# Performance work log

Measured on AMD Instinct MI355X. Metric: run time of the kernel, lower is better.

The kernel has to match this reference:

```python
import jax, jax.numpy as jnp
import numpy as np

N = 50000; E = 800000; G = 64
HID = 128; HEADS = 4; HC = HID // HEADS
L = 3; RESID_FREQ = 2
EPS = 1e-5; SLOPE = 0.2


def setup_inputs() -> dict:
    key = jax.random.key(0)
    ks = jax.random.split(key, 16)
    s = 1.0 / np.sqrt(HID)
    f = jnp.float32
    return {
        "x": jax.random.normal(ks[0], (N, HID), f),
        "edge_index": jax.random.randint(ks[1], (2, E), 0, N, dtype=jnp.int32),
        "batch": jnp.sort(jax.random.randint(ks[2], (N,), 0, G, dtype=jnp.int32)),
        "w_in1": jax.random.normal(ks[3], (HID, HID), f) * s,
        "b_in1": jnp.zeros((HID,), f),
        "w_in2": jax.random.normal(ks[4], (HID, HID), f) * s,
        "b_in2": jnp.zeros((HID,), f),
        "gat_w": jax.random.normal(ks[5], (L, HID, HID), f) * s,
        "gat_att_src": jax.random.normal(ks[6], (L, HEADS, HC), f) * s,
        "gat_att_dst": jax.random.normal(ks[7], (L, HEADS, HC), f) * s,
        "gat_b": jnp.zeros((L, HID), f),
        "gcn_w": jax.random.normal(ks[8], (L, HID, HID), f) * s,
        "gcn_b": jnp.zeros((L, HID), f),
        "norm_w": jnp.ones((L, HID), f),
        "norm_b": jnp.zeros((L, HID), f),
        "norm_ms": jnp.ones((L, HID), f),
        "skip_w": jax.random.normal(ks[9], (L, HID, HID), f) * s,
        "skip_b": jnp.zeros((L, HID), f),
        "w_h1": jax.random.normal(ks[10], (HID, HID), f) * s,
        "b_h1": jnp.zeros((HID,), f),
        "w_h2": jax.random.normal(ks[11], (HID, HID // 2), f) * s,
        "b_h2": jnp.zeros((HID // 2,), f),
        "w_h3": jax.random.normal(ks[12], (HID // 2, 1), f) * s,
        "b_h3": jnp.zeros((1,), f),
        "edge_w_param": jnp.ones((1,), f),
    }


def _gat(x, src, dst, w, a_src, a_dst, b):
    # PyG GATConv (eval): lin -> per-edge additive attention -> edge softmax over dst -> scatter-sum
    h = (x @ w).reshape(N, HEADS, HC)
    sc_src = jnp.sum(h * a_src, axis=-1)  # [N, H]
    sc_dst = jnp.sum(h * a_dst, axis=-1)
    alpha = jax.nn.leaky_relu(sc_src[src] + sc_dst[dst], SLOPE)  # [Ef, H]
    amax = jax.ops.segment_max(alpha, dst, num_segments=N)  # every node has a self-loop
    ex = jnp.exp(alpha - amax[dst])
    denom = jax.ops.segment_sum(ex, dst, num_segments=N)
    coef = ex / (denom[dst] + 1e-16)
    out = jax.ops.segment_sum(h[src] * coef[:, :, None], dst, num_segments=N)
    return out.reshape(N, HID) + b


def _gcn(x, src, dst, ew, w, b):
    # PyG GCNConv with improved=True (self-loop weight 2.0 already in ew): sym-normalized SpMM
    deg = jax.ops.segment_sum(ew, dst, num_segments=N)
    dinv = jnp.where(deg > 0, jax.lax.rsqrt(deg), 0.0)
    norm = dinv[src] * ew * dinv[dst]
    h = x @ w
    return jax.ops.segment_sum(h[src] * norm[:, None], dst, num_segments=N) + b


def _graph_norm(x, batch, w, b, ms):
    cnt = jax.ops.segment_sum(jnp.ones((N, 1), x.dtype), batch, num_segments=G)
    cnt = jnp.maximum(cnt, 1.0)
    mean = jax.ops.segment_sum(x, batch, num_segments=G) / cnt
    out = x - mean[batch] * ms
    var = jax.ops.segment_sum(out * out, batch, num_segments=G) / cnt
    return out / jnp.sqrt(var[batch] + EPS) * w + b


def reference(x, edge_index, batch, w_in1, b_in1, w_in2, b_in2, gat_w, gat_att_src,
              gat_att_dst, gat_b, gcn_w, gcn_b, norm_w, norm_b, norm_ms, skip_w,
              skip_b, w_h1, b_h1, w_h2, b_h2, w_h3, b_h3, edge_w_param):
    # undirected: concat reversed edges; then self-loops (added by both GAT and GCN convs)
    loop = jnp.arange(N, dtype=edge_index.dtype)
    src = jnp.concatenate([edge_index[0], edge_index[1], loop])
    dst = jnp.concatenate([edge_index[1], edge_index[0], loop])
    ew = jnp.concatenate([
        edge_w_param[0] * jnp.ones((2 * E,), x.dtype),
        2.0 * jnp.ones((N,), x.dtype),  # improved=True self-loop fill value
    ])
    h = jax.nn.relu(x @ w_in1 + b_in1) @ w_in2 + b_in2
    for i in range(L):
        prev = h
        g1 = _gat(h, src, dst, gat_w[i], gat_att_src[i], gat_att_dst[i], gat_b[i])
        g2 = _gcn(h, src, dst, ew, gcn_w[i], gcn_b[i])
        h = jax.nn.elu(_graph_norm(g1 + g2, batch, norm_w[i], norm_b[i], norm_ms[i]))
        if i % RESID_FREQ == 0:
            h = h + prev @ skip_w[i] + skip_b[i]
    p = jax.nn.relu(h @ w_h1 + b_h1)
    p = jax.nn.relu(p @ w_h2 + b_h2)
    return jax.nn.sigmoid(p @ w_h3 + b_h3).reshape(-1)
```

## Files before the change

### kernel.cpp

```cpp
#include <hip/hip_runtime.h>
#include <hip/hip_fp16.h>

typedef unsigned int uint;
typedef unsigned short ushort;
typedef __attribute__((ext_vector_type(8))) short short8;
typedef __attribute__((ext_vector_type(4))) float f32x4;

#define N_NODES 50000
#define N_EDGES 800000
#define ETOT    (2 * N_EDGES + N_NODES)
#define NG      64
#define NBKT    256
#define MAXB    10240
#define EPB     8192
#define NBK1    ((ETOT + EPB - 1) / EPB)
#define GSTR    320

__device__ __forceinline__ short f2bf(float f) {
  uint u = __float_as_uint(f);
  u += 0x7fffu + ((u >> 16) & 1u);
  return (short)(u >> 16);
}
__device__ __forceinline__ float bf2f(short s) {
  return __uint_as_float(((uint)(ushort)s) << 16);
}
__device__ __forceinline__ uint packbf(float a, float b) {
  return (uint)(ushort)f2bf(a) | ((uint)(ushort)f2bf(b) << 16);
}
__device__ __forceinline__ uint pkh2(float a, float b) {
  __half2 h = __floats2half2_rn(a, b);
  return *(uint*)&h;
}
__device__ __forceinline__ float2 uph2(uint u) {
  __half2 h = *(__half2*)&u;
  return __half22float2(h);
}

__global__ __launch_bounds__(256) void bucket_k(const int* __restrict__ ei,
                                                int* __restrict__ gfill,
                                                uint* __restrict__ est) {
  __shared__ int hist[NBKT];
  __shared__ int cursor[NBKT];
  const int tid = threadIdx.x;
  hist[tid] = 0;
  __syncthreads();
  const int e0 = blockIdx.x * EPB;
#pragma unroll 4
  for (int i = 0; i < EPB / 256; ++i) {
    int e = e0 + i * 256 + tid;
    if (e < ETOT) {
      int d;
      if (e < N_EDGES)          d = ei[N_EDGES + e];
      else if (e < 2 * N_EDGES) d = ei[e - N_EDGES];
      else                      d = e - 2 * N_EDGES;
      atomicAdd(&hist[d >> 8], 1);
    }
  }
  __syncthreads();
  cursor[tid] = atomicAdd(&gfill[tid], hist[tid]);
  __syncthreads();
#pragma unroll 4
  for (int i = 0; i < EPB / 256; ++i) {
    int e = e0 + i * 256 + tid;
    if (e < ETOT) {
      int s, d, fl = 0;
      if (e < N_EDGES)          { s = ei[e];           d = ei[N_EDGES + e]; }
      else if (e < 2 * N_EDGES) { s = ei[e];           d = ei[e - N_EDGES]; }
      else                      { s = e - 2 * N_EDGES; d = s; fl = 1; }
      int b = d >> 8;
      int slot = atomicAdd(&cursor[b], 1);
      est[(size_t)b * MAXB + slot] = (uint)s | ((uint)(d & 255) << 16) | ((uint)fl << 24);
    }
  }
}

__global__ __launch_bounds__(256) void bktscan_k(const int* __restrict__ gfill,
                                                 int* __restrict__ bktbase) {
  __shared__ int wsum[4];
  int tid = threadIdx.x, lane = tid & 63, wid = tid >> 6;
  int v = gfill[tid];
  int x = v;
#pragma unroll
  for (int d = 1; d < 64; d <<= 1) {
    int t = __shfl_up(x, d, 64);
    if (lane >= d) x += t;
  }
  if (lane == 63) wsum[wid] = x;
  __syncthreads();
  int woff = 0;
#pragma unroll
  for (int j = 0; j < 4; ++j) if (j < wid) woff += wsum[j];
  bktbase[tid] = woff + x - v;
}

__global__ __launch_bounds__(256) void group_k(const int* __restrict__ gfill,
                                               const int* __restrict__ bktbase,
                                               const uint* __restrict__ est,
                                               const float* __restrict__ ewp,
                                               int* __restrict__ csrc,
                                               int* __restrict__ rbeg,
                                               int* __restrict__ rend,
                                               float* __restrict__ dinv) {
  __shared__ int hist[NBKT];
  __shared__ int cursor[NBKT];
  __shared__ int wsum[4];
  const int b = blockIdx.x;
  const int tid = threadIdx.x;
  const int cnt = gfill[b];
  const int gb = bktbase[b];
  hist[tid] = 0;
  __syncthreads();
  const uint* basep = est + (size_t)b * MAXB;
  for (int i = tid; i < cnt; i += 256)
    atomicAdd(&hist[(basep[i] >> 16) & 255], 1);
  __syncthreads();
  int v = hist[tid];
  int lane = tid & 63, wid = tid >> 6;
  int x = v;
#pragma unroll
  for (int d = 1; d < 64; d <<= 1) {
    int t = __shfl_up(x, d, 64);
    if (lane >= d) x += t;
  }
  if (lane == 63) wsum[wid] = x;
  __syncthreads();
  int woff = 0;
#pragma unroll
  for (int j = 0; j < 4; ++j) if (j < wid) woff += wsum[j];
  int excl = woff + x - v;
  cursor[tid] = excl;
  int node = b * 256 + tid;
  if (node < N_NODES) {
    rbeg[node] = gb + excl;
    rend[node] = gb + excl + v;
    float deg = ewp[0] * (float)(v - 1) + 2.0f;
    dinv[node] = (deg > 0.f) ? rsqrtf(deg) : 0.f;
  }
  __syncthreads();
  for (int i = tid; i < cnt; i += 256) {
    uint en = basep[i];
    int dlow = (en >> 16) & 255;
    int slot = atomicAdd(&cursor[dlow], 1);
    csrc[gb + slot] = (int)(en & 0xffffu) | (int)((en >> 24) << 31);
  }
}

__global__ __launch_bounds__(128) void gcnt_k(const int* __restrict__ batch,
                                              int* __restrict__ gcnt) {
  __shared__ int lb[NG + 1];
  int g = threadIdx.x;
  if (g <= NG) {
    int lo = 0, hi = N_NODES;
    while (lo < hi) {
      int mid = (lo + hi) >> 1;
      if (batch[mid] < g) lo = mid + 1; else hi = mid;
    }
    lb[g] = lo;
  }
  __syncthreads();
  if (g < NG) gcnt[g] = lb[g + 1] - lb[g];
}

__global__ __launch_bounds__(256) void convx_k(const float* __restrict__ x,
                                               short* __restrict__ xb) {
  int i = (blockIdx.x * 256 + threadIdx.x) * 4;
  float4 v = *(const float4*)(x + i);
  *(uint2*)(xb + i) = make_uint2(packbf(v.x, v.y), packbf(v.z, v.w));
}

__global__ __launch_bounds__(256) void prep_k(const float* __restrict__ w_in1,
                                              const float* __restrict__ w_in2,
                                              const float* __restrict__ gat_w,
                                              const float* __restrict__ gcn_w,
                                              const float* __restrict__ skip_w,
                                              const float* __restrict__ w_h1,
                                              const float* __restrict__ w_h2,
                                              short* __restrict__ WT0,
                                              short* __restrict__ WT1,
                                              short* __restrict__ WTL2,
                                              short* __restrict__ WTS,
                                              short* __restrict__ WTH1,
                                              short* __restrict__ WTH2) {
  int mat = blockIdx.x >> 2, qr = blockIdx.x & 3;
  const float* src; short* dst; int ncol = 128, dstride = 128, doff = 0;
  switch (mat) {
    case 0:  src = w_in1; dst = WT0; break;
    case 1:  src = w_in2; dst = WT1; break;
    case 2: case 3: case 4:
      src = gat_w + (size_t)(mat - 2) * 16384; dst = WTL2 + (size_t)(mat - 2) * 32768;
      dstride = 256; break;
    case 5: case 6: case 7:
      src = gcn_w + (size_t)(mat - 5) * 16384; dst = WTL2 + (size_t)(mat - 5) * 32768;
      dstride = 256; doff = 128; break;
    case 8:  src = skip_w;             dst = WTS;         break;
    case 9:  src = skip_w + 2 * 16384; dst = WTS + 16384; break;
    case 10: src = w_h1; dst = WTH1; break;
    default: src = w_h2; dst = WTH2; ncol = 64; break;
  }
  int total = 128 * ncol, chunk = total / 4;
  for (int d = qr * chunk + threadIdx.x; d < (qr + 1) * chunk; d += 256) {
    int col = d >> 7, k = d & 127;
    dst[col * dstride + doff + k] = f2bf(src[k * ncol + col]);
  }
}

__global__ __launch_bounds__(256) void attprep_k(const float* __restrict__ gat_w,
                                                 const float* __restrict__ asrc,
                                                 const float* __restrict__ adst,
                                                 const float* __restrict__ gat_b,
                                                 const float* __restrict__ gcn_b,
                                                 short* __restrict__ ATTW,
                                                 float* __restrict__ BSUM) {
  const int tid = threadIdx.x;
  for (int t = tid; t < 3072; t += 256) {
    int l = t >> 10, rem = t & 1023;
    int r = rem >> 7, k = rem & 127;
    int hd = r & 3;
    const float* av = (r < 4) ? (asrc + l * 128 + hd * 32) : (adst + l * 128 + hd * 32);
    const float* wrow = gat_w + (size_t)l * 16384 + k * 128 + hd * 32;
    float s = 0.f;
#pragma unroll
    for (int c = 0; c < 32; ++c) s = fmaf(wrow[c], av[c], s);
    ATTW[(size_t)l * 2048 + r * 128 + k] = f2bf(s);
  }
  for (int t = tid; t < 3072; t += 256)
    ATTW[(size_t)(t >> 10) * 2048 + 1024 + (t & 1023)] = 0;
  for (int t = tid; t < 384; t += 256) {
    int l = t >> 7, c = t & 127;
    BSUM[t] = gat_b[l * 128 + c] + gcn_b[l * 128 + c];
  }
}

template <int NCOL, int RELU, int ADD, int F32OUT>
__global__ __launch_bounds__(256) void bgemm_k(const short* __restrict__ A,
                                               const short* __restrict__ WT,
                                               const float* __restrict__ bias,
                                               const float* __restrict__ addsrc,
                                               short* __restrict__ outb,
                                               float* __restrict__ outf,
                                               int astr, int M) {
  constexpr int NT = NCOL / 16;
  const int lane = threadIdx.x & 63;
  const int wid = threadIdx.x >> 6;
  const int mbase = blockIdx.x * 64 + wid * 16;
  const int l15 = lane & 15, q = lane >> 4;
  int arow = mbase + l15; if (arow > M - 1) arow = M - 1;
  const short* ap = A + (size_t)arow * 128 + q * 8;
  const short* bp = WT + (size_t)l15 * 128 + q * 8;
  f32x4 acc[NT];
#pragma unroll
  for (int t = 0; t < NT; ++t) acc[t] = (f32x4)0.f;
#pragma unroll
  for (int c = 0; c < 4; ++c) {
    short8 av = *(const short8*)(ap + c * 32);
#pragma unroll
    for (int t = 0; t < NT; ++t) {
      short8 bv = *(const short8*)(bp + (size_t)t * 16 * 128 + c * 32);
      acc[t] = __builtin_amdgcn_mfma_f32_16x16x32_bf16(av, bv, acc[t], 0, 0, 0);
    }
  }
#pragma unroll
  for (int t = 0; t < NT; ++t) {
    int col = t * 16 + l15;
    float bb = bias ? bias[col] : 0.f;
#pragma unroll
    for (int r = 0; r < 4; ++r) {
      int row = mbase + q * 4 + r;
      if (row < M) {
        float v = acc[t][r] + bb;
        if (ADD) v += addsrc[(size_t)row * astr + col];
        if (RELU) v = v > 0.f ? v : 0.f;
        if (F32OUT) outf[(size_t)row * NCOL + col] = v;
        else        outb[(size_t)row * NCOL + col] = f2bf(v);
      }
    }
  }
}

__global__ __launch_bounds__(256) void coef_k(const float* __restrict__ sc,
                                              const int* __restrict__ rbeg,
                                              const int* __restrict__ rend,
                                              const int* __restrict__ cs,
                                              const float* __restrict__ dinv,
                                              const float* __restrict__ ewp,
                                              uint* __restrict__ COEF) {
  const int n = blockIdx.x * 4 + (threadIdx.x >> 6);
  const int l = threadIdx.x & 63;
  const float ew0 = ewp[0];
  const float dn = dinv[n];
  const f32x4 sdv = *(const f32x4*)(sc + n * 16 + 4);
  const int beg = rbeg[n], end = rend[n];
  float den0 = 0.f, den1 = 0.f, den2 = 0.f, den3 = 0.f;
  for (int e = beg + l; e < end; e += 64) {
    int raw = cs[e];
    int s = raw & 0x7fffffff;
    float w = (raw < 0) ? 2.0f : ew0;
    f32x4 ssv = *(const f32x4*)(sc + (size_t)s * 16);
    float a0 = ssv[0] + sdv[0]; a0 = fmaxf(a0, 0.2f * a0);
    float a1 = ssv[1] + sdv[1]; a1 = fmaxf(a1, 0.2f * a1);
    float a2 = ssv[2] + sdv[2]; a2 = fmaxf(a2, 0.2f * a2);
    float a3 = ssv[3] + sdv[3]; a3 = fmaxf(a3, 0.2f * a3);
    float e0 = __expf(a0), e1 = __expf(a1), e2 = __expf(a2), e3 = __expf(a3);
    den0 += e0; den1 += e1; den2 += e2; den3 += e3;
    float c2 = dinv[s] * w * dn;
    uint* cp = COEF + (size_t)e * 3;
    cp[0] = pkh2(e0, e1);
    cp[1] = pkh2(e2, e3);
    __half hc = __float2half(c2);
    cp[2] = (uint)(*(ushort*)&hc) | ((uint)s << 16);
  }
#pragma unroll
  for (int off = 32; off; off >>= 1) {
    den0 += __shfl_xor(den0, off, 64);
    den1 += __shfl_xor(den1, off, 64);
    den2 += __shfl_xor(den2, off, 64);
    den3 += __shfl_xor(den3, off, 64);
  }
  float i0 = 1.0f / (den0 + 1e-16f), i1 = 1.0f / (den1 + 1e-16f);
  float i2 = 1.0f / (den2 + 1e-16f), i3 = 1.0f / (den3 + 1e-16f);
  for (int e = beg + l; e < end; e += 64) {
    uint* cp = COEF + (size_t)e * 3;
    float2 p01 = uph2(cp[0]);
    float2 p23 = uph2(cp[1]);
    cp[0] = pkh2(p01.x * i0, p01.y * i1);
    cp[1] = pkh2(p23.x * i2, p23.y * i3);
  }
}

__global__ __launch_bounds__(256) void agg_k(const short* __restrict__ h,
                                             const uint* __restrict__ COEF,
                                             const int* __restrict__ rbeg,
                                             const int* __restrict__ rend,
                                             short* __restrict__ A) {
  const int n = blockIdx.x * 4 + (threadIdx.x >> 6);
  const int l = threadIdx.x & 63;
  const int sub = l >> 5;
  const int f4 = l & 31;
  const int beg = rbeg[n], end = rend[n];
  float ag[4][4], ac[4];
#pragma unroll
  for (int hd = 0; hd < 4; ++hd)
#pragma unroll
    for (int i = 0; i < 4; ++i) ag[hd][i] = 0.f;
#pragma unroll
  for (int i = 0; i < 4; ++i) ac[i] = 0.f;
  for (int e0 = beg; e0 < end; e0 += 2) {
    int e = e0 + sub;
    int ec = (e < end) ? e : ETOT;
    const uint* cp = COEF + (size_t)ec * 3;
    uint c0 = cp[0], c1 = cp[1], c2w = cp[2];
    int s = (int)(c2w >> 16);
    float2 p01 = uph2(c0);
    float2 p23 = uph2(c1);
    ushort hc = (ushort)(c2w & 0xffffu);
    float c2 = __half2float(*(__half*)&hc);
    uint2 u = *(const uint2*)(h + (size_t)s * 128 + f4 * 4);
    float v0 = __uint_as_float(u.x << 16);
    float v1 = __uint_as_float(u.x & 0xffff0000u);
    float v2 = __uint_as_float(u.y << 16);
    float v3 = __uint_as_float(u.y & 0xffff0000u);
    ag[0][0] = fmaf(p01.x, v0, ag[0][0]); ag[0][1] = fmaf(p01.x, v1, ag[0][1]);
    ag[0][2] = fmaf(p01.x, v2, ag[0][2]); ag[0][3] = fmaf(p01.x, v3, ag[0][3]);
    ag[1][0] = fmaf(p01.y, v0, ag[1][0]); ag[1][1] = fmaf(p01.y, v1, ag[1][1]);
    ag[1][2] = fmaf(p01.y, v2, ag[1][2]); ag[1][3] = fmaf(p01.y, v3, ag[1][3]);
    ag[2][0] = fmaf(p23.x, v0, ag[2][0]); ag[2][1] = fmaf(p23.x, v1, ag[2][1]);
    ag[2][2] = fmaf(p23.x, v2, ag[2][2]); ag[2][3] = fmaf(p23.x, v3, ag[2][3]);
    ag[3][0] = fmaf(p23.y, v0, ag[3][0]); ag[3][1] = fmaf(p23.y, v1, ag[3][1]);
    ag[3][2] = fmaf(p23.y, v2, ag[3][2]); ag[3][3] = fmaf(p23.y, v3, ag[3][3]);
    ac[0] = fmaf(c2, v0, ac[0]); ac[1] = fmaf(c2, v1, ac[1]);
    ac[2] = fmaf(c2, v2, ac[2]); ac[3] = fmaf(c2, v3, ac[3]);
  }
#pragma unroll
  for (int hd = 0; hd < 4; ++hd)
#pragma unroll
    for (int i = 0; i < 4; ++i) ag[hd][i] += __shfl_xor(ag[hd][i], 32);
#pragma unroll
  for (int i = 0; i < 4; ++i) ac[i] += __shfl_xor(ac[i], 32);
  short* base = A + (size_t)n * 640;
  if (sub == 0) {
#pragma unroll
    for (int hd = 0; hd < 2; ++hd) {
      *(uint2*)(base + hd * 128 + f4 * 4) =
          make_uint2(packbf(ag[hd][0], ag[hd][1]), packbf(ag[hd][2], ag[hd][3]));
    }
    *(uint2*)(base + 512 + f4 * 4) =
        make_uint2(packbf(ac[0], ac[1]), packbf(ac[2], ac[3]));
  } else {
#pragma unroll
    for (int hd = 2; hd < 4; ++hd) {
      *(uint2*)(base + hd * 128 + f4 * 4) =
          make_uint2(packbf(ag[hd][0], ag[hd][1]), packbf(ag[hd][2], ag[hd][3]));
    }
  }
}

__global__ __launch_bounds__(256) void aggproj_k(const short* A,
                                                 const short* __restrict__ WT,
                                                 const float* __restrict__ bsum,
                                                 float* G, int M) {
  const int lane = threadIdx.x & 63;
  const int wid = threadIdx.x >> 6;
  const int mbase = blockIdx.x * 64 + wid * 16;
  const int l15 = lane & 15, q = lane >> 4;
  int arow = mbase + l15; if (arow > M - 1) arow = M - 1;
  const short* ap = A + (size_t)arow * 640 + q * 8;
  const short* bp = WT + (size_t)l15 * 256 + q * 8;
  f32x4 acc[8];
#pragma unroll
  for (int t = 0; t < 8; ++t) acc[t] = (f32x4)0.f;
  short8 avg[4];
#pragma unroll
  for (int c = 0; c < 4; ++c) avg[c] = *(const short8*)(ap + 512 + c * 32);
#pragma unroll
  for (int hd = 0; hd < 4; ++hd) {
    short8 avh[4];
#pragma unroll
    for (int c = 0; c < 4; ++c) avh[c] = *(const short8*)(ap + hd * 128 + c * 32);
#pragma unroll
    for (int tt = 0; tt < 2; ++tt) {
      int t = hd * 2 + tt;
      const short* bpt = bp + (size_t)t * 16 * 256;
#pragma unroll
      for (int c = 0; c < 4; ++c) {
        short8 bv = *(const short8*)(bpt + c * 32);
        acc[t] = __builtin_amdgcn_mfma_f32_16x16x32_bf16(avh[c], bv, acc[t], 0, 0, 0);
      }
#pragma unroll
      for (int c = 0; c < 4; ++c) {
        short8 bv = *(const short8*)(bpt + 128 + c * 32);
        acc[t] = __builtin_amdgcn_mfma_f32_16x16x32_bf16(avg[c], bv, acc[t], 0, 0, 0);
      }
    }
  }
#pragma unroll
  for (int t = 0; t < 8; ++t) {
    int col = t * 16 + l15;
    float bb = bsum[col];
#pragma unroll
    for (int r = 0; r < 4; ++r) {
      int row = mbase + q * 4 + r;
      if (row < M) G[(size_t)row * GSTR + col] = acc[t][r] + bb;
    }
  }
}

__global__ __launch_bounds__(256) void stats_k(const float* __restrict__ g,
                                               const int* __restrict__ batch,
                                               float* __restrict__ gsum) {
  int c = threadIdx.x & 127;
  int half = threadIdx.x >> 7;
  int nb = blockIdx.x * 16;
  float s = 0.f, q = 0.f;
  int curb = -1;
  for (int i = half; i < 16; i += 2) {
    int n = nb + i;
    int b = batch[n];
    if (b != curb) {
      if (curb >= 0) {
        atomicAdd(&gsum[curb * 256 + c], s);
        atomicAdd(&gsum[curb * 256 + 128 + c], q);
      }
      curb = b; s = 0.f; q = 0.f;
    }
    float v = g[(size_t)n * GSTR + c];
    s += v;
    q = fmaf(v, v, q);
  }
  if (curb >= 0) {
    atomicAdd(&gsum[curb * 256 + c], s);
    atomicAdd(&gsum[curb * 256 + 128 + c], q);
  }
}

template <int OUTBF16>
__global__ __launch_bounds__(256) void normelu_k(float* __restrict__ g,
                                                 const int* __restrict__ batch,
                                                 const float* __restrict__ gsum,
                                                 const int* __restrict__ gcnt,
                                                 const float* __restrict__ nw,
                                                 const float* __restrict__ nb_,
                                                 const float* __restrict__ nms,
                                                 short* __restrict__ outb) {
  int n = blockIdx.x * 2 + (threadIdx.x >> 7);
  int c = threadIdx.x & 127;
  int b = batch[n];
  float cntf = fmaxf((float)gcnt[b], 1.0f);
  float inv = 1.0f / cntf;
  float mean = gsum[b * 256 + c] * inv;
  float msq  = gsum[b * 256 + 128 + c] * inv;
  float ms = nms[c];
  float var = fmaxf(msq - (2.0f * ms - ms * ms) * mean * mean, 0.f);
  float v = g[(size_t)n * GSTR + c];
  float o = (v - mean * ms) * rsqrtf(var + 1e-5f) * nw[c] + nb_[c];
  o = (o > 0.f) ? o : (__expf(o) - 1.0f);
  if (OUTBF16) outb[(size_t)n * 128 + c] = f2bf(o);
  else         g[(size_t)n * GSTR + c] = o;
}

__global__ __launch_bounds__(256) void head3_k(const short* __restrict__ p2,
                                               const float* __restrict__ w3,
                                               const float* __restrict__ b3,
                                               float* __restrict__ out) {
  int n = blockIdx.x * 4 + (threadIdx.x >> 6);
  int k = threadIdx.x & 63;
  float v = bf2f(p2[(size_t)n * 64 + k]) * w3[k];
#pragma unroll
  for (int off = 32; off; off >>= 1) v += __shfl_down(v, off, 64);
  if (k == 0) out[n] = 1.0f / (1.0f + __expf(-(v + b3[0])));
}

extern "C" void kernel_launch(void* const* d_in, const int* in_sizes, int n_in,
                              void* d_out, int out_size, void* d_ws, size_t ws_size,
                              hipStream_t stream) {
  const float* x      = (const float*)d_in[0];
  const int*   ei     = (const int*)d_in[1];
  const int*   batch  = (const int*)d_in[2];
  const float* w_in1  = (const float*)d_in[3];
  const float* b_in1  = (const float*)d_in[4];
  const float* w_in2  = (const float*)d_in[5];
  const float* b_in2  = (const float*)d_in[6];
  const float* gat_w  = (const float*)d_in[7];
  const float* gat_as = (const float*)d_in[8];
  const float* gat_ad = (const float*)d_in[9];
  const float* gat_b  = (const float*)d_in[10];
  const float* gcn_w  = (const float*)d_in[11];
  const float* gcn_b  = (const float*)d_in[12];
  const float* norm_w = (const float*)d_in[13];
  const float* norm_b = (const float*)d_in[14];
  const float* norm_ms= (const float*)d_in[15];
  const float* skip_w = (const float*)d_in[16];
  const float* skip_b = (const float*)d_in[17];
  const float* w_h1   = (const float*)d_in[18];
  const float* b_h1   = (const float*)d_in[19];
  const float* w_h2   = (const float*)d_in[20];
  const float* b_h2   = (const float*)d_in[21];
  const float* w_h3   = (const float*)d_in[22];
  const float* b_h3   = (const float*)d_in[23];
  const float* ewp    = (const float*)d_in[24];
  float* out = (float*)d_out;

  char* p = (char*)d_ws;
  const size_t NBH = (size_t)N_NODES * 128 * sizeof(short);
  short* B0   = (short*)p; p += NBH;
  short* B1   = (short*)p; p += NBH;
  short* MEGA = (short*)p; p += (size_t)N_NODES * 640 * sizeof(short);
  float* G    = (float*)MEGA;
  uint*  EST  = (uint*)MEGA;
  float* SC   = (float*)p; p += (size_t)N_NODES * 16 * sizeof(float);
  int*   CSRC = (int*)p;   p += (size_t)ETOT * sizeof(int);
  uint*  COEF = (uint*)p;  p += (size_t)(ETOT + 1) * 3 * sizeof(uint);
  int*   RBEG = (int*)p;   p += (size_t)N_NODES * sizeof(int);
  int*   REND = (int*)p;   p += (size_t)N_NODES * sizeof(int);
  char*  zbase = p;
  int*   GFILL= (int*)p;   p += (size_t)NBKT * sizeof(int);
  float* GSUM = (float*)p; p += (size_t)3 * NG * 256 * sizeof(float);
  size_t znb  = (size_t)((char*)p - zbase);
  int*   BKTB = (int*)p;   p += (size_t)NBKT * sizeof(int);
  int*   GCNT = (int*)p;   p += (size_t)NG * sizeof(int);
  float* DINV = (float*)p; p += (size_t)N_NODES * sizeof(float);
  short* WT0  = (short*)p; p += 16384 * sizeof(short);
  short* WT1  = (short*)p; p += 16384 * sizeof(short);
  short* WTL2 = (short*)p; p += 3 * 32768 * sizeof(short);
  short* WTS  = (short*)p; p += 2 * 16384 * sizeof(short);
  short* WTH1 = (short*)p; p += 16384 * sizeof(short);
  short* WTH2 = (short*)p; p += 8192 * sizeof(short);
  short* ATTW = (short*)p; p += 3 * 2048 * sizeof(short);
  float* BSUM = (float*)p; p += 3 * 128 * sizeof(float);

  const int GB = (N_NODES + 63) / 64;

  hipMemsetAsync(zbase, 0, znb, stream);
  hipMemsetAsync(COEF + (size_t)ETOT * 3, 0, 12, stream);
  bucket_k<<<NBK1, 256, 0, stream>>>(ei, GFILL, EST);
  bktscan_k<<<1, 256, 0, stream>>>(GFILL, BKTB);
  group_k<<<196, 256, 0, stream>>>(GFILL, BKTB, EST, ewp, CSRC, RBEG, REND, DINV);
  gcnt_k<<<1, 128, 0, stream>>>(batch, GCNT);
  convx_k<<<(N_NODES * 128) / 1024, 256, 0, stream>>>(x, B0);
  prep_k<<<48, 256, 0, stream>>>(w_in1, w_in2, gat_w, gcn_w, skip_w, w_h1, w_h2,
                                 WT0, WT1, WTL2, WTS, WTH1, WTH2);
  attprep_k<<<1, 256, 0, stream>>>(gat_w, gat_as, gat_ad, gat_b, gcn_b, ATTW, BSUM);

  bgemm_k<128, 1, 0, 0><<<GB, 256, 0, stream>>>(B0, WT0, b_in1, nullptr, B1, nullptr, 0, N_NODES);
  bgemm_k<128, 0, 0, 0><<<GB, 256, 0, stream>>>(B1, WT1, b_in2, nullptr, B0, nullptr, 0, N_NODES);

  short* h = B0;
  for (int i = 0; i < 3; ++i) {
    short* hn = (h == B0) ? B1 : B0;
    float* gsum_i = GSUM + (size_t)i * NG * 256;
    bgemm_k<16, 0, 0, 1><<<GB, 256, 0, stream>>>(h, ATTW + (size_t)i * 2048,
                                                 nullptr, nullptr, nullptr, SC, 0, N_NODES);
    coef_k<<<N_NODES / 4, 256, 0, stream>>>(SC, RBEG, REND, CSRC, DINV, ewp, COEF);
    agg_k<<<N_NODES / 4, 256, 0, stream>>>(h, COEF, RBEG, REND, MEGA);
    aggproj_k<<<GB, 256, 0, stream>>>(MEGA, WTL2 + (size_t)i * 32768,
                                      BSUM + i * 128, G, N_NODES);
    stats_k<<<N_NODES / 16, 256, 0, stream>>>(G, batch, gsum_i);
    if (i == 1) {
      normelu_k<1><<<N_NODES / 2, 256, 0, stream>>>(G, batch, gsum_i, GCNT,
          norm_w + (size_t)i * 128, norm_b + (size_t)i * 128, norm_ms + (size_t)i * 128,
          hn);
    } else {
      normelu_k<0><<<N_NODES / 2, 256, 0, stream>>>(G, batch, gsum_i, GCNT,
          norm_w + (size_t)i * 128, norm_b + (size_t)i * 128, norm_ms + (size_t)i * 128,
          nullptr);
      const short* wts = WTS + (size_t)(i == 0 ? 0 : 1) * 16384;
      bgemm_k<128, 0, 1, 0><<<GB, 256, 0, stream>>>(h, wts, skip_b + (size_t)i * 128,
                                                    G, hn, nullptr, GSTR, N_NODES);
    }
    h = hn;
  }

  bgemm_k<128, 1, 0, 0><<<GB, 256, 0, stream>>>(h, WTH1, b_h1, nullptr, B0, nullptr, 0, N_NODES);
  bgemm_k<64, 1, 0, 0><<<GB, 256, 0, stream>>>(B0, WTH2, b_h2, nullptr, MEGA, nullptr, 0, N_NODES);
  head3_k<<<N_NODES / 4, 256, 0, stream>>>(MEGA, w_h3, b_h3, out);
}
```

Measured before the change: 984.4 us.

## Fuse edge-coefficient computation into aggregation and store graph-norm intermediates in bf16

Merges the separate coef_k pass into agg_k: each wave computes unnormalized attention exponents and GCN weights for 64 edges at a time into shared memory, aggregates them, and applies the softmax denominator at the end. This removes the COEF global buffer and its write/read/rewrite traffic plus one launch per layer. The projected pre-norm output G also switches from fp32 to bf16, the normalized result goes to a separate bf16 buffer, and stats/normelu are widened to two channels per thread. The cost is some precision loss in the norm inputs and softmax exponents that are no longer max-subtracted, though the code before also skipped that subtraction.

Result: faster. 878.1 us (-10.8%).

```diff
diff --git a/kernel.cpp b/kernel.cpp
--- a/kernel.cpp
+++ b/kernel.cpp
@@ -14,7 +14,7 @@
 #define MAXB    10240
 #define EPB     8192
 #define NBK1    ((ETOT + EPB - 1) / EPB)
-#define GSTR    320
+#define AROW    640
 
 __device__ __forceinline__ short f2bf(float f) {
   uint u = __float_as_uint(f);
@@ -235,10 +235,9 @@
 __global__ __launch_bounds__(256) void bgemm_k(const short* __restrict__ A,
                                                const short* __restrict__ WT,
                                                const float* __restrict__ bias,
-                                               const float* __restrict__ addsrc,
+                                               const short* __restrict__ addsrc,
                                                short* __restrict__ outb,
-                                               float* __restrict__ outf,
-                                               int astr, int M) {
+                                               float* __restrict__ outf, int M) {
   constexpr int NT = NCOL / 16;
   const int lane = threadIdx.x & 63;
   const int wid = threadIdx.x >> 6;
@@ -268,7 +267,7 @@
       int row = mbase + q * 4 + r;
       if (row < M) {
         float v = acc[t][r] + bb;
-        if (ADD) v += addsrc[(size_t)row * astr + col];
+        if (ADD) v += bf2f(addsrc[(size_t)row * 128 + col]);
         if (RELU) v = v > 0.f ? v : 0.f;
         if (F32OUT) outf[(size_t)row * NCOL + col] = v;
         else        outb[(size_t)row * NCOL + col] = f2bf(v);
@@ -277,66 +276,25 @@
   }
 }
 
-__global__ __launch_bounds__(256) void coef_k(const float* __restrict__ sc,
-                                              const int* __restrict__ rbeg,
-                                              const int* __restrict__ rend,
-                                              const int* __restrict__ cs,
-                                              const float* __restrict__ dinv,
-                                              const float* __restrict__ ewp,
-                                              uint* __restrict__ COEF) {
+__global__ __launch_bounds__(256) void agg_k(const short* __restrict__ h,
+                                             const float* __restrict__ sc,
+                                             const int* __restrict__ rbeg,
+                                             const int* __restrict__ rend,
+                                             const int* __restrict__ cs,
+                                             const float* __restrict__ dinv,
+                                             const float* __restrict__ ewp,
+                                             short* __restrict__ A) {
+  __shared__ uint lco[4][64][3];
   const int n = blockIdx.x * 4 + (threadIdx.x >> 6);
+  const int wv = threadIdx.x >> 6;
   const int l = threadIdx.x & 63;
+  const int sub = l >> 5;
+  const int f4 = l & 31;
   const float ew0 = ewp[0];
   const float dn = dinv[n];
   const f32x4 sdv = *(const f32x4*)(sc + n * 16 + 4);
   const int beg = rbeg[n], end = rend[n];
-  float den0 = 0.f, den1 = 0.f, den2 = 0.f, den3 = 0.f;
-  for (int e = beg + l; e < end; e += 64) {
-    int raw = cs[e];
-    int s = raw & 0x7fffffff;
-    float w = (raw < 0) ? 2.0f : ew0;
-    f32x4 ssv = *(const f32x4*)(sc + (size_t)s * 16);
-    float a0 = ssv[0] + sdv[0]; a0 = fmaxf(a0, 0.2f * a0);
-    float a1 = ssv[1] + sdv[1]; a1 = fmaxf(a1, 0.2f * a1);
-    float a2 = ssv[2] + sdv[2]; a2 = fmaxf(a2, 0.2f * a2);
-    float a3 = ssv[3] + sdv[3]; a3 = fmaxf(a3, 0.2f * a3);
-    float e0 = __expf(a0), e1 = __expf(a1), e2 = __expf(a2), e3 = __expf(a3);
-    den0 += e0; den1 += e1; den2 += e2; den3 += e3;
-    float c2 = dinv[s] * w * dn;
-    uint* cp = COEF + (size_t)e * 3;
-    cp[0] = pkh2(e0, e1);
-    cp[1] = pkh2(e2, e3);
-    __half hc = __float2half(c2);
-    cp[2] = (uint)(*(ushort*)&hc) | ((uint)s << 16);
-  }
-#pragma unroll
-  for (int off = 32; off; off >>= 1) {
-    den0 += __shfl_xor(den0, off, 64);
-    den1 += __shfl_xor(den1, off, 64);
-    den2 += __shfl_xor(den2, off, 64);
-    den3 += __shfl_xor(den3, off, 64);
-  }
-  float i0 = 1.0f / (den0 + 1e-16f), i1 = 1.0f / (den1 + 1e-16f);
-  float i2 = 1.0f / (den2 + 1e-16f), i3 = 1.0f / (den3 + 1e-16f);
-  for (int e = beg + l; e < end; e += 64) {
-    uint* cp = COEF + (size_t)e * 3;
-    float2 p01 = uph2(cp[0]);
-    float2 p23 = uph2(cp[1]);
-    cp[0] = pkh2(p01.x * i0, p01.y * i1);
-    cp[1] = pkh2(p23.x * i2, p23.y * i3);
-  }
-}
-
-__global__ __launch_bounds__(256) void agg_k(const short* __restrict__ h,
-                                             const uint* __restrict__ COEF,
-                                             const int* __restrict__ rbeg,
-                                             const int* __restrict__ rend,
-                                             short* __restrict__ A) {
-  const int n = blockIdx.x * 4 + (threadIdx.x >> 6);
-  const int l = threadIdx.x & 63;
-  const int sub = l >> 5;
-  const int f4 = l & 31;
-  const int beg = rbeg[n], end = rend[n];
+  float den[4] = {0.f, 0.f, 0.f, 0.f};
   float ag[4][4], ac[4];
 #pragma unroll
   for (int hd = 0; hd < 4; ++hd)
@@ -344,52 +302,97 @@
     for (int i = 0; i < 4; ++i) ag[hd][i] = 0.f;
 #pragma unroll
   for (int i = 0; i < 4; ++i) ac[i] = 0.f;
-  for (int e0 = beg; e0 < end; e0 += 2) {
-    int e = e0 + sub;
-    int ec = (e < end) ? e : ETOT;
-    const uint* cp = COEF + (size_t)ec * 3;
-    uint c0 = cp[0], c1 = cp[1], c2w = cp[2];
-    int s = (int)(c2w >> 16);
-    float2 p01 = uph2(c0);
-    float2 p23 = uph2(c1);
-    ushort hc = (ushort)(c2w & 0xffffu);
-    float c2 = __half2float(*(__half*)&hc);
-    uint2 u = *(const uint2*)(h + (size_t)s * 128 + f4 * 4);
-    float v0 = __uint_as_float(u.x << 16);
-    float v1 = __uint_as_float(u.x & 0xffff0000u);
-    float v2 = __uint_as_float(u.y << 16);
-    float v3 = __uint_as_float(u.y & 0xffff0000u);
-    ag[0][0] = fmaf(p01.x, v0, ag[0][0]); ag[0][1] = fmaf(p01.x, v1, ag[0][1]);
-    ag[0][2] = fmaf(p01.x, v2, ag[0][2]); ag[0][3] = fmaf(p01.x, v3, ag[0][3]);
-    ag[1][0] = fmaf(p01.y, v0, ag[1][0]); ag[1][1] = fmaf(p01.y, v1, ag[1][1]);
-    ag[1][2] = fmaf(p01.y, v2, ag[1][2]); ag[1][3] = fmaf(p01.y, v3, ag[1][3]);
-    ag[2][0] = fmaf(p23.x, v0, ag[2][0]); ag[2][1] = fmaf(p23.x, v1, ag[2][1]);
-    ag[2][2] = fmaf(p23.x, v2, ag[2][2]); ag[2][3] = fmaf(p23.x, v3, ag[2][3]);
-    ag[3][0] = fmaf(p23.y, v0, ag[3][0]); ag[3][1] = fmaf(p23.y, v1, ag[3][1]);
-    ag[3][2] = fmaf(p23.y, v2, ag[3][2]); ag[3][3] = fmaf(p23.y, v3, ag[3][3]);
-    ac[0] = fmaf(c2, v0, ac[0]); ac[1] = fmaf(c2, v1, ac[1]);
-    ac[2] = fmaf(c2, v2, ac[2]); ac[3] = fmaf(c2, v3, ac[3]);
+
+  for (int c0 = beg; c0 < end; c0 += 64) {
+    const int nc = min(64, end - c0);
+    {
+      uint w0 = 0, w1 = 0, w2 = 0;
+      int e = c0 + l;
+      if (e < end) {
+        int raw = cs[e];
+        int s = raw & 0x7fffffff;
+        float w = (raw < 0) ? 2.0f : ew0;
+        f32x4 ssv = *(const f32x4*)(sc + (size_t)s * 16);
+        float a0 = ssv[0] + sdv[0]; a0 = fmaxf(a0, 0.2f * a0);
+        float a1 = ssv[1] + sdv[1]; a1 = fmaxf(a1, 0.2f * a1);
+        float a2 = ssv[2] + sdv[2]; a2 = fmaxf(a2, 0.2f * a2);
+        float a3 = ssv[3] + sdv[3]; a3 = fmaxf(a3, 0.2f * a3);
+        float e0 = __expf(a0), e1 = __expf(a1);
+        float e2 = __expf(a2), e3 = __expf(a3);
+        den[0] += e0; den[1] += e1; den[2] += e2; den[3] += e3;
+        float c2 = dinv[s] * w * dn;
+        w0 = pkh2(e0, e1);
+        w1 = pkh2(e2, e3);
+        __half hc = __float2half(c2);
+        w2 = (uint)(*(ushort*)&hc) | ((uint)s << 16);
+      }
+      lco[wv][l][0] = w0;
+      lco[wv][l][1] = w1;
+      lco[wv][l][2] = w2;
+    }
+    const int pairs = (nc + 1) & ~1;
+#pragma unroll 2
+    for (int j = sub; j < pairs; j += 2) {
+      uint c0w = lco[wv][j][0];
+      uint c1w = lco[wv][j][1];
+      uint c2w = lco[wv][j][2];
+      int s = (int)(c2w >> 16);
+      float2 p01 = uph2(c0w);
+      float2 p23 = uph2(c1w);
+      ushort hc = (ushort)(c2w & 0xffffu);
+      float c2 = __half2float(*(__half*)&hc);
+      uint2 u = *(const uint2*)(h + (size_t)s * 128 + f4 * 4);
+      float v0 = __uint_as_float(u.x << 16);
+      float v1 = __uint_as_float(u.x & 0xffff0000u);
+      float v2 = __uint_as_float(u.y << 16);
+      float v3 = __uint_as_float(u.y & 0xffff0000u);
+      ag[0][0] = fmaf(p01.x, v0, ag[0][0]); ag[0][1] = fmaf(p01.x, v1, ag[0][1]);
+      ag[0][2] = fmaf(p01.x, v2, ag[0][2]); ag[0][3] = fmaf(p01.x, v3, ag[0][3]);
+      ag[1][0] = fmaf(p01.y, v0, ag[1][0]); ag[1][1] = fmaf(p01.y, v1, ag[1][1]);
+      ag[1][2] = fmaf(p01.y, v2, ag[1][2]); ag[1][3] = fmaf(p01.y, v3, ag[1][3]);
+      ag[2][0] = fmaf(p23.x, v0, ag[2][0]); ag[2][1] = fmaf(p23.x, v1, ag[2][1]);
+      ag[2][2] = fmaf(p23.x, v2, ag[2][2]); ag[2][3] = fmaf(p23.x, v3, ag[2][3]);
+      ag[3][0] = fmaf(p23.y, v0, ag[3][0]); ag[3][1] = fmaf(p23.y, v1, ag[3][1]);
+      ag[3][2] = fmaf(p23.y, v2, ag[3][2]); ag[3][3] = fmaf(p23.y, v3, ag[3][3]);
+      ac[0] = fmaf(c2, v0, ac[0]); ac[1] = fmaf(c2, v1, ac[1]);
+      ac[2] = fmaf(c2, v2, ac[2]); ac[3] = fmaf(c2, v3, ac[3]);
+    }
+  }
+
+#pragma unroll
+  for (int off = 1; off < 64; off <<= 1) {
+    den[0] += __shfl_xor(den[0], off, 64);
+    den[1] += __shfl_xor(den[1], off, 64);
+    den[2] += __shfl_xor(den[2], off, 64);
+    den[3] += __shfl_xor(den[3], off, 64);
   }
 #pragma unroll
   for (int hd = 0; hd < 4; ++hd)
 #pragma unroll
-    for (int i = 0; i < 4; ++i) ag[hd][i] += __shfl_xor(ag[hd][i], 32);
-#pragma unroll
-  for (int i = 0; i < 4; ++i) ac[i] += __shfl_xor(ac[i], 32);
-  short* base = A + (size_t)n * 640;
+    for (int i = 0; i < 4; ++i) ag[hd][i] += __shfl_xor(ag[hd][i], 32, 64);
+#pragma unroll
+  for (int i = 0; i < 4; ++i) ac[i] += __shfl_xor(ac[i], 32, 64);
+
+  float inv[4] = {1.0f / (den[0] + 1e-16f), 1.0f / (den[1] + 1e-16f),
+                  1.0f / (den[2] + 1e-16f), 1.0f / (den[3] + 1e-16f)};
+  short* base = A + (size_t)n * AROW;
   if (sub == 0) {
 #pragma unroll
     for (int hd = 0; hd < 2; ++hd) {
+      float iv = inv[hd];
       *(uint2*)(base + hd * 128 + f4 * 4) =
-          make_uint2(packbf(ag[hd][0], ag[hd][1]), packbf(ag[hd][2], ag[hd][3]));
+          make_uint2(packbf(ag[hd][0] * iv, ag[hd][1] * iv),
+                     packbf(ag[hd][2] * iv, ag[hd][3] * iv));
     }
     *(uint2*)(base + 512 + f4 * 4) =
         make_uint2(packbf(ac[0], ac[1]), packbf(ac[2], ac[3]));
   } else {
 #pragma unroll
     for (int hd = 2; hd < 4; ++hd) {
+      float iv = inv[hd];
       *(uint2*)(base + hd * 128 + f4 * 4) =
-          make_uint2(packbf(ag[hd][0], ag[hd][1]), packbf(ag[hd][2], ag[hd][3]));
+          make_uint2(packbf(ag[hd][0] * iv, ag[hd][1] * iv),
+                     packbf(ag[hd][2] * iv, ag[hd][3] * iv));
     }
   }
 }
@@ -397,13 +400,13 @@
 __global__ __launch_bounds__(256) void aggproj_k(const short* A,
                                                  const short* __restrict__ WT,
                                                  const float* __restrict__ bsum,
-                                                 float* G, int M) {
+                                                 short* GB, int M) {
   const int lane = threadIdx.x & 63;
   const int wid = threadIdx.x >> 6;
   const int mbase = blockIdx.x * 64 + wid * 16;
   const int l15 = lane & 15, q = lane >> 4;
   int arow = mbase + l15; if (arow > M - 1) arow = M - 1;
-  const short* ap = A + (size_t)arow * 640 + q * 8;
+  const short* ap = A + (size_t)arow * AROW + q * 8;
   const short* bp = WT + (size_t)l15 * 256 + q * 8;
   f32x4 acc[8];
 #pragma unroll
@@ -439,41 +442,46 @@
 #pragma unroll
     for (int r = 0; r < 4; ++r) {
       int row = mbase + q * 4 + r;
-      if (row < M) G[(size_t)row * GSTR + col] = acc[t][r] + bb;
-    }
-  }
-}
-
-__global__ __launch_bounds__(256) void stats_k(const float* __restrict__ g,
+      if (row < M) GB[(size_t)row * AROW + col] = f2bf(acc[t][r] + bb);
+    }
+  }
+}
+
+__global__ __launch_bounds__(256) void stats_k(const short* __restrict__ gb,
                                                const int* __restrict__ batch,
                                                float* __restrict__ gsum) {
-  int c = threadIdx.x & 127;
-  int half = threadIdx.x >> 7;
+  int c2 = threadIdx.x & 63;
+  int qr = threadIdx.x >> 6;
   int nb = blockIdx.x * 16;
-  float s = 0.f, q = 0.f;
+  float s0 = 0.f, s1 = 0.f, q0 = 0.f, q1 = 0.f;
   int curb = -1;
-  for (int i = half; i < 16; i += 2) {
+  for (int i = qr; i < 16; i += 4) {
     int n = nb + i;
     int b = batch[n];
     if (b != curb) {
       if (curb >= 0) {
-        atomicAdd(&gsum[curb * 256 + c], s);
-        atomicAdd(&gsum[curb * 256 + 128 + c], q);
+        atomicAdd(&gsum[curb * 256 + 2 * c2], s0);
+        atomicAdd(&gsum[curb * 256 + 2 * c2 + 1], s1);
+        atomicAdd(&gsum[curb * 256 + 128 + 2 * c2], q0);
+        atomicAdd(&gsum[curb * 256 + 128 + 2 * c2 + 1], q1);
       }
-      curb = b; s = 0.f; q = 0.f;
-    }
-    float v = g[(size_t)n * GSTR + c];
-    s += v;
-    q = fmaf(v, v, q);
+      curb = b; s0 = s1 = q0 = q1 = 0.f;
+    }
+    uint u = *(const uint*)(gb + (size_t)n * AROW + 2 * c2);
+    float v0 = __uint_as_float(u << 16);
+    float v1 = __uint_as_float(u & 0xffff0000u);
+    s0 += v0; q0 = fmaf(v0, v0, q0);
+    s1 += v1; q1 = fmaf(v1, v1, q1);
   }
   if (curb >= 0) {
-    atomicAdd(&gsum[curb * 256 + c], s);
-    atomicAdd(&gsum[curb * 256 + 128 + c], q);
-  }
-}
-
-template <int OUTBF16>
-__global__ __launch_bounds__(256) void normelu_k(float* __restrict__ g,
+    atomicAdd(&gsum[curb * 256 + 2 * c2], s0);
+    atomicAdd(&gsum[curb * 256 + 2 * c2 + 1], s1);
+    atomicAdd(&gsum[curb * 256 + 128 + 2 * c2], q0);
+    atomicAdd(&gsum[curb * 256 + 128 + 2 * c2 + 1], q1);
+  }
+}
+
+__global__ __launch_bounds__(256) void normelu_k(const short* __restrict__ gb,
                                                  const int* __restrict__ batch,
                                                  const float* __restrict__ gsum,
                                                  const int* __restrict__ gcnt,
@@ -481,20 +489,25 @@
                                                  const float* __restrict__ nb_,
                                                  const float* __restrict__ nms,
                                                  short* __restrict__ outb) {
-  int n = blockIdx.x * 2 + (threadIdx.x >> 7);
-  int c = threadIdx.x & 127;
+  int n = blockIdx.x * 4 + (threadIdx.x >> 6);
+  int c2 = threadIdx.x & 63;
   int b = batch[n];
   float cntf = fmaxf((float)gcnt[b], 1.0f);
-  float inv = 1.0f / cntf;
-  float mean = gsum[b * 256 + c] * inv;
-  float msq  = gsum[b * 256 + 128 + c] * inv;
-  float ms = nms[c];
-  float var = fmaxf(msq - (2.0f * ms - ms * ms) * mean * mean, 0.f);
-  float v = g[(size_t)n * GSTR + c];
-  float o = (v - mean * ms) * rsqrtf(var + 1e-5f) * nw[c] + nb_[c];
-  o = (o > 0.f) ? o : (__expf(o) - 1.0f);
-  if (OUTBF16) outb[(size_t)n * 128 + c] = f2bf(o);
-  else         g[(size_t)n * GSTR + c] = o;
+  float cinv = 1.0f / cntf;
+  uint u = *(const uint*)(gb + (size_t)n * AROW + 2 * c2);
+  float o[2];
+#pragma unroll
+  for (int k = 0; k < 2; ++k) {
+    int c = 2 * c2 + k;
+    float mean = gsum[b * 256 + c] * cinv;
+    float msq  = gsum[b * 256 + 128 + c] * cinv;
+    float ms = nms[c];
+    float var = fmaxf(msq - (2.0f * ms - ms * ms) * mean * mean, 0.f);
+    float v = (k == 0) ? __uint_as_float(u << 16) : __uint_as_float(u & 0xffff0000u);
+    float t = (v - mean * ms) * rsqrtf(var + 1e-5f) * nw[c] + nb_[c];
+    o[k] = (t > 0.f) ? t : (__expf(t) - 1.0f);
+  }
+  *(uint*)(outb + (size_t)n * 128 + 2 * c2) = packbf(o[0], o[1]);
 }
 
 __global__ __launch_bounds__(256) void head3_k(const short* __restrict__ p2,
@@ -543,12 +556,12 @@
   const size_t NBH = (size_t)N_NODES * 128 * sizeof(short);
   short* B0   = (short*)p; p += NBH;
   short* B1   = (short*)p; p += NBH;
-  short* MEGA = (short*)p; p += (size_t)N_NODES * 640 * sizeof(short);
-  float* G    = (float*)MEGA;
+  short* NRM  = (short*)p; p += NBH;
+  short* MEGA = (short*)p; p += (size_t)N_NODES * AROW * sizeof(short);
+  short* GB   = MEGA;
   uint*  EST  = (uint*)MEGA;
   float* SC   = (float*)p; p += (size_t)N_NODES * 16 * sizeof(float);
   int*   CSRC = (int*)p;   p += (size_t)ETOT * sizeof(int);
-  uint*  COEF = (uint*)p;  p += (size_t)(ETOT + 1) * 3 * sizeof(uint);
   int*   RBEG = (int*)p;   p += (size_t)N_NODES * sizeof(int);
   int*   REND = (int*)p;   p += (size_t)N_NODES * sizeof(int);
   char*  zbase = p;
@@ -567,10 +580,9 @@
   short* ATTW = (short*)p; p += 3 * 2048 * sizeof(short);
   float* BSUM = (float*)p; p += 3 * 128 * sizeof(float);
 
-  const int GB = (N_NODES + 63) / 64;
+  const int GB_ = (N_NODES + 63) / 64;
 
   hipMemsetAsync(zbase, 0, znb, stream);
-  hipMemsetAsync(COEF + (size_t)ETOT * 3, 0, 12, stream);
   bucket_k<<<NBK1, 256, 0, stream>>>(ei, GFILL, EST);
   bktscan_k<<<1, 256, 0, stream>>>(GFILL, BKTB);
   group_k<<<196, 256, 0, stream>>>(GFILL, BKTB, EST, ewp, CSRC, RBEG, REND, DINV);
@@ -580,36 +592,35 @@
                                  WT0, WT1, WTL2, WTS, WTH1, WTH2);
   attprep_k<<<1, 256, 0, stream>>>(gat_w, gat_as, gat_ad, gat_b, gcn_b, ATTW, BSUM);
 
-  bgemm_k<128, 1, 0, 0><<<GB, 256, 0, stream>>>(B0, WT0, b_in1, nullptr, B1, nullptr, 0, N_NODES);
-  bgemm_k<128, 0, 0, 0><<<GB, 256, 0, stream>>>(B1, WT1, b_in2, nullptr, B0, nullptr, 0, N_NODES);
+  bgemm_k<128, 1, 0, 0><<<GB_, 256, 0, stream>>>(B0, WT0, b_in1, nullptr, B1, nullptr, N_NODES);
+  bgemm_k<128, 0, 0, 0><<<GB_, 256, 0, stream>>>(B1, WT1, b_in2, nullptr, B0, nullptr, N_NODES);
 
   short* h = B0;
   for (int i = 0; i < 3; ++i) {
     short* hn = (h == B0) ? B1 : B0;
     float* gsum_i = GSUM + (size_t)i * NG * 256;
-    bgemm_k<16, 0, 0, 1><<<GB, 256, 0, stream>>>(h, ATTW + (size_t)i * 2048,
-                                                 nullptr, nullptr, nullptr, SC, 0, N_NODES);
-    coef_k<<<N_NODES / 4, 256, 0, stream>>>(SC, RBEG, REND, CSRC, DINV, ewp, COEF);
-    agg_k<<<N_NODES / 4, 256, 0, stream>>>(h, COEF, RBEG, REND, MEGA);
-    aggproj_k<<<GB, 256, 0, stream>>>(MEGA, WTL2 + (size_t)i * 32768,
-                                      BSUM + i * 128, G, N_NODES);
-    stats_k<<<N_NODES / 16, 256, 0, stream>>>(G, batch, gsum_i);
+    bgemm_k<16, 0, 0, 1><<<GB_, 256, 0, stream>>>(h, ATTW + (size_t)i * 2048,
+                                                  nullptr, nullptr, nullptr, SC, N_NODES);
+    agg_k<<<N_NODES / 4, 256, 0, stream>>>(h, SC, RBEG, REND, CSRC, DINV, ewp, MEGA);
+    aggproj_k<<<GB_, 256, 0, stream>>>(MEGA, WTL2 + (size_t)i * 32768,
+                                       BSUM + i * 128, GB, N_NODES);
+    stats_k<<<N_NODES / 16, 256, 0, stream>>>(GB, batch, gsum_i);
     if (i == 1) {
-      normelu_k<1><<<N_NODES / 2, 256, 0, stream>>>(G, batch, gsum_i, GCNT,
+      normelu_k<<<N_NODES / 4, 256, 0, stream>>>(GB, batch, gsum_i, GCNT,
           norm_w + (size_t)i * 128, norm_b + (size_t)i * 128, norm_ms + (size_t)i * 128,
           hn);
     } else {
-      normelu_k<0><<<N_NODES / 2, 256, 0, stream>>>(G, batch, gsum_i, GCNT,
+      normelu_k<<<N_NODES / 4, 256, 0, stream>>>(GB, batch, gsum_i, GCNT,
           norm_w + (size_t)i * 128, norm_b + (size_t)i * 128, norm_ms + (size_t)i * 128,
-          nullptr);
+          NRM);
       const short* wts = WTS + (size_t)(i == 0 ? 0 : 1) * 16384;
-      bgemm_k<128, 0, 1, 0><<<GB, 256, 0, stream>>>(h, wts, skip_b + (size_t)i * 128,
-                                                    G, hn, nullptr, GSTR, N_NODES);
+      bgemm_k<128, 0, 1, 0><<<GB_, 256, 0, stream>>>(h, wts, skip_b + (size_t)i * 128,
+                                                     NRM, hn, nullptr, N_NODES);
     }
     h = hn;
   }
 
-  bgemm_k<128, 1, 0, 0><<<GB, 256, 0, stream>>>(h, WTH1, b_h1, nullptr, B0, nullptr, 0, N_NODES);
-  bgemm_k<64, 1, 0, 0><<<GB, 256, 0, stream>>>(B0, WTH2, b_h2, nullptr, MEGA, nullptr, 0, N_NODES);
+  bgemm_k<128, 1, 0, 0><<<GB_, 256, 0, stream>>>(h, WTH1, b_h1, nullptr, B0, nullptr, N_NODES);
+  bgemm_k<64, 1, 0, 0><<<GB_, 256, 0, stream>>>(B0, WTH2, b_h2, nullptr, MEGA, nullptr, N_NODES);
   head3_k<<<N_NODES / 4, 256, 0, stream>>>(MEGA, w_h3, b_h3, out);
 }
```
